# Optimization experiments

Hardware: AMD Instinct MI355X
Metric: run time of the kernel (lower is better)

The kernel has to match this reference:

```python
import jax, jax.numpy as jnp
import numpy as np
import math

S, B, D = 2048, 8, 256
HEADS = 8
DPROJ = 128
DFF = 1024
DH = DPROJ // HEADS  # 16


def _layernorm(x, g, b, eps=1e-5):
    mu = jnp.mean(x, axis=-1, keepdims=True)
    var = jnp.mean((x - mu) ** 2, axis=-1, keepdims=True)
    return (x - mu) * jax.lax.rsqrt(var + eps) * g + b


def setup_inputs() -> dict:
    key = jax.random.key(0)
    ks = jax.random.split(key, 16)
    s = 0.02
    return {
        "src": jax.random.normal(ks[0], (S, B, D), dtype=jnp.float32),
        "Wq": jax.random.normal(ks[1], (D, DPROJ), dtype=jnp.float32) * s,
        "bq": jnp.zeros((DPROJ,), dtype=jnp.float32),
        "Wk": jax.random.normal(ks[2], (D, DPROJ), dtype=jnp.float32) * s,
        "bk": jnp.zeros((DPROJ,), dtype=jnp.float32),
        "Wv": jax.random.normal(ks[3], (D, DPROJ), dtype=jnp.float32) * s,
        "bv": jnp.zeros((DPROJ,), dtype=jnp.float32),
        "Wo": jax.random.normal(ks[4], (DPROJ, D), dtype=jnp.float32) * s,
        "ln1_g": jnp.ones((D,), dtype=jnp.float32),
        "ln1_b": jnp.zeros((D,), dtype=jnp.float32),
        "W1": jax.random.normal(ks[5], (D, DFF), dtype=jnp.float32) * s,
        "b1": jnp.zeros((DFF,), dtype=jnp.float32),
        "W2": jax.random.normal(ks[6], (DFF, D), dtype=jnp.float32) * s,
        "b2": jnp.zeros((D,), dtype=jnp.float32),
        "ln2_g": jnp.ones((D,), dtype=jnp.float32),
        "ln2_b": jnp.zeros((D,), dtype=jnp.float32),
    }


def reference(src, Wq, bq, Wk, bk, Wv, bv, Wo, ln1_g, ln1_b, W1, b1, W2, b2, ln2_g, ln2_b):
    # src: (S, B, D)
    q = src @ Wq + bq  # (S, B, DPROJ)
    k = src @ Wk + bk
    v = src @ Wv + bv

    # _reshape_to_batches: (S, B, h*dh) -> (S, B*h, dh), then sdpa moves batch first
    def split_heads(x):
        return jnp.transpose(x.reshape(S, B * HEADS, DH), (1, 0, 2))  # (B*h, S, dh)

    qh, kh, vh = split_heads(q), split_heads(k), split_heads(v)
    scores = jnp.einsum('bid,bjd->bij', qh, kh) / math.sqrt(DH)  # (B*h, S, S)
    attn = jax.nn.softmax(scores, axis=-1)
    ctx = jnp.einsum('bij,bjd->bid', attn, vh)  # (B*h, S, dh)

    # _reshape_from_batches: (B*h, S, dh) -> (S, B, DPROJ)
    ctx = jnp.transpose(ctx, (1, 0, 2)).reshape(S, B, DPROJ)
    y = ctx @ Wo  # (S, B, D), no bias

    x = _layernorm(src + y, ln1_g, ln1_b)
    ffn = jax.nn.relu(x @ W1 + b1) @ W2 + b2
    return _layernorm(x + ffn, ln2_g, ln2_b)
```

## Files before the change

### kernel.cpp

```cpp
#include <hip/hip_runtime.h>
#include <math.h>

#define SLEN 2048
#define BATCH 8
#define DMODEL 256
#define HEADS 8
#define DPROJ 128
#define DFF 1024
#define DH 16
#define MROWS (SLEN*BATCH)

typedef unsigned short u16;
typedef unsigned int u32;
typedef __attribute__((ext_vector_type(8))) short short8;
typedef __attribute__((ext_vector_type(4))) float f32x4;
typedef __attribute__((ext_vector_type(4))) unsigned short u16x4;

__device__ __forceinline__ u16 f2bf(float x) {
    union { float f; u32 u; } v; v.f = x;
    u32 r = v.u + 0x7FFFu + ((v.u >> 16) & 1u);
    return (u16)(r >> 16);
}
__device__ __forceinline__ float bf2f(u16 h) {
    union { u32 u; float f; } v; v.u = ((u32)h) << 16;
    return v.f;
}
__device__ __forceinline__ float fexp2(float x) { return __builtin_amdgcn_exp2f(x); }
__device__ __forceinline__ u32 pack_bf(float lo, float hi) {
    union { float f; u32 u; } a, b; a.f = lo; b.f = hi;
    return __builtin_amdgcn_perm(b.u, a.u, 0x07060302u);
}
__device__ __forceinline__ void gld16(const u16* g, u16* l) {
    __builtin_amdgcn_global_load_lds(
        (const __attribute__((address_space(1))) void*)g,
        (__attribute__((address_space(3))) void*)l, 16, 0, 0);
}

__global__ void prep_kernel(const float* __restrict__ src, u16* __restrict__ srcb,
                            const float* __restrict__ Wq, const float* __restrict__ Wk,
                            const float* __restrict__ Wv, const float* __restrict__ Wo,
                            const float* __restrict__ W1, const float* __restrict__ W2,
                            u16* __restrict__ WqT, u16* __restrict__ WkT,
                            u16* __restrict__ WvT, u16* __restrict__ WoT,
                            u16* __restrict__ W1T, u16* __restrict__ W2T) {
    if (blockIdx.x < 4096) {
        int idx = (blockIdx.x * 256 + threadIdx.x) * 4;
        float4 v = *(const float4*)(src + idx);
        u16x4 o;
        o.x = f2bf(v.x); o.y = f2bf(v.y); o.z = f2bf(v.z); o.w = f2bf(v.w);
        *(u16x4*)(srcb + idx) = o;
        return;
    }
    int i = (blockIdx.x - 4096) * 256 + threadIdx.x;
    if (i < 32768) {
        int n = i >> 8, k = i & 255;
        WqT[i] = f2bf(Wq[k * 128 + n]);
    } else if (i < 65536) {
        int j = i - 32768; int n = j >> 8, k = j & 255;
        WkT[j] = f2bf(Wk[k * 128 + n]);
    } else if (i < 98304) {
        int j = i - 65536; int n = j >> 8, k = j & 255;
        WvT[j] = f2bf(Wv[k * 128 + n]);
    } else if (i < 131072) {
        int j = i - 98304; int n = j >> 7, k = j & 127;
        WoT[j] = f2bf(Wo[k * 256 + n]);
    } else if (i < 393216) {
        int j = i - 131072; int n = j >> 8, k = j & 255;
        W1T[j] = f2bf(W1[k * 1024 + n]);
    } else if (i < 655360) {
        int j = i - 393216; int n = j >> 10, k = j & 1023;
        W2T[j] = f2bf(W2[k * 256 + n]);
    }
}

template<int BN, bool RELU, bool HAS_BIAS, bool OUT_BF16>
__global__ void mfma_gemm(const u16* __restrict__ A, const u16* __restrict__ BT,
                          const float* __restrict__ bias, void* __restrict__ Cout,
                          int M, int N, int K) {
    constexpr int NJ = BN / 32;
    __shared__ __align__(16) u16 As[128 * 32];
    __shared__ __align__(16) u16 Bs[BN * 32];
    const int tid = threadIdx.x;
    const int row0 = blockIdx.x * 128;
    const int col0 = blockIdx.y * BN;
    const int w = tid >> 6, l = tid & 63;
    const int wr = (w & 1) * 64, wc = (w >> 1) * (BN / 2);
    const int lcol = l & 15, lrow = (l >> 4) * 4, g = l >> 4;
    const int sl = l >> 2;
    const int swc = ((l & 3) ^ (sl & 3)) * 8;
    const int fsw = (g ^ (lcol & 3)) * 8;

    const u16* Ag0 = A + (size_t)(row0 + 16 * w + sl) * K + swc;
    const u16* Ag1 = Ag0 + (size_t)64 * K;
    const u16* Bg0 = BT + (size_t)(col0 + 16 * w + sl) * K + swc;
    const u16* Bg1 = Bg0 + (size_t)64 * K;
    u16* lA0 = As + (16 * w) * 32;
    u16* lA1 = As + (16 * w + 64) * 32;
    u16* lB0 = Bs + (16 * w) * 32;
    u16* lB1 = Bs + (16 * w + 64) * 32;

    f32x4 acc[4][NJ] = {};
    for (int k0 = 0; k0 < K; k0 += 32) {
        gld16(Ag0 + k0, lA0);
        gld16(Ag1 + k0, lA1);
        gld16(Bg0 + k0, lB0);
        if (BN == 128) gld16(Bg1 + k0, lB1);
        __syncthreads();
        short8 af[4], bf[NJ];
        #pragma unroll
        for (int i = 0; i < 4; ++i)
            af[i] = *(const short8*)(As + (wr + i * 16 + lcol) * 32 + fsw);
        #pragma unroll
        for (int j = 0; j < NJ; ++j)
            bf[j] = *(const short8*)(Bs + (wc + j * 16 + lcol) * 32 + fsw);
        #pragma unroll
        for (int i = 0; i < 4; ++i)
            #pragma unroll
            for (int j = 0; j < NJ; ++j)
                acc[i][j] = __builtin_amdgcn_mfma_f32_16x16x32_bf16(
                    af[i], bf[j], acc[i][j], 0, 0, 0);
        __syncthreads();
    }
    float bv[NJ];
    #pragma unroll
    for (int j = 0; j < NJ; ++j)
        bv[j] = HAS_BIAS ? bias[col0 + wc + j * 16 + lcol] : 0.f;
    #pragma unroll
    for (int i = 0; i < 4; ++i) {
        #pragma unroll
        for (int r = 0; r < 4; ++r) {
            size_t grow = row0 + wr + i * 16 + lrow + r;
            #pragma unroll
            for (int j = 0; j < NJ; ++j) {
                int gcol = col0 + wc + j * 16 + lcol;
                float c = acc[i][j][r] + bv[j];
                if (RELU) c = fmaxf(c, 0.f);
                if (OUT_BF16) ((u16*)Cout)[grow * N + gcol] = f2bf(c);
                else          ((float*)Cout)[grow * N + gcol] = c;
            }
        }
    }
}

__global__ void qkv_mfma(const u16* __restrict__ A,
                         const u16* __restrict__ WqT, const u16* __restrict__ WkT,
                         const u16* __restrict__ WvT,
                         const float* __restrict__ bq, const float* __restrict__ bk,
                         const float* __restrict__ bv,
                         u16* __restrict__ qhp, u16* __restrict__ khp,
                         u16* __restrict__ vhb) {
    const int which = blockIdx.z;
    const u16* BT   = which == 0 ? WqT : (which == 1 ? WkT : WvT);
    const float* bs = which == 0 ? bq : (which == 1 ? bk : bv);
    const float scale = which == 0 ? 0.25f * 1.44269504f : 1.0f;
    __shared__ __align__(16) u16 As[128 * 32];
    __shared__ __align__(16) u16 Bs[128 * 32];
    const int tid = threadIdx.x;
    const int row0 = blockIdx.x * 128;
    const int w = tid >> 6, l = tid & 63;
    const int wr = (w & 1) * 64, wc = (w >> 1) * 64;
    const int lcol = l & 15, lrow = (l >> 4) * 4, g = l >> 4;
    const int sl = l >> 2;
    const int swc = ((l & 3) ^ (sl & 3)) * 8;
    const int fsw = (g ^ (lcol & 3)) * 8;

    const u16* Ag0 = A + (size_t)(row0 + 16 * w + sl) * DMODEL + swc;
    const u16* Ag1 = Ag0 + (size_t)64 * DMODEL;
    const u16* Bg0 = BT + (size_t)(16 * w + sl) * DMODEL + swc;
    const u16* Bg1 = Bg0 + (size_t)64 * DMODEL;
    u16* lA0 = As + (16 * w) * 32;
    u16* lA1 = As + (16 * w + 64) * 32;
    u16* lB0 = Bs + (16 * w) * 32;
    u16* lB1 = Bs + (16 * w + 64) * 32;

    f32x4 acc[4][4] = {};
    for (int k0 = 0; k0 < DMODEL; k0 += 32) {
        gld16(Ag0 + k0, lA0);
        gld16(Ag1 + k0, lA1);
        gld16(Bg0 + k0, lB0);
        gld16(Bg1 + k0, lB1);
        __syncthreads();
        short8 af[4], bf[4];
        #pragma unroll
        for (int i = 0; i < 4; ++i)
            af[i] = *(const short8*)(As + (wr + i * 16 + lcol) * 32 + fsw);
        #pragma unroll
        for (int j = 0; j < 4; ++j)
            bf[j] = *(const short8*)(Bs + (wc + j * 16 + lcol) * 32 + fsw);
        #pragma unroll
        for (int i = 0; i < 4; ++i)
            #pragma unroll
            for (int j = 0; j < 4; ++j)
                acc[i][j] = __builtin_amdgcn_mfma_f32_16x16x32_bf16(
                    af[i], bf[j], acc[i][j], 0, 0, 0);
        __syncthreads();
    }
    #pragma unroll
    for (int i = 0; i < 4; ++i) {
        #pragma unroll
        for (int r = 0; r < 4; ++r) {
            int grow = row0 + wr + i * 16 + lrow + r;
            int b = grow & 7, s = grow >> 3;
            #pragma unroll
            for (int j = 0; j < 4; ++j) {
                int gcol = wc + j * 16 + lcol;
                int h = gcol >> 4, d = gcol & 15;
                float c = acc[i][j][r] + bs[gcol];
                if (which == 2) {
                    vhb[((size_t)(b * 8 + h) * SLEN + s) * 16 + d] = f2bf(c);
                } else {
                    u16* base = (which == 0 ? qhp : khp)
                              + ((size_t)(b * 8 + h) * SLEN + s) * 32;
                    base[d] = f2bf(c * scale);
                    base[d + 16] = 0;
                }
            }
        }
    }
}

__global__ void transpose_v(const u16* __restrict__ vhb, u16* __restrict__ vT) {
    __shared__ u16 T[128 * 24];
    const int bh = blockIdx.y;
    const int c0 = blockIdx.x * 128;
    const int t = threadIdx.x;
    {
        int key = t >> 1, half = t & 1;
        *(uint4*)(T + key * 24 + half * 8) =
            *(const uint4*)(vhb + ((size_t)bh * SLEN + c0 + key) * 16 + half * 8);
    }
    __syncthreads();
    int d = t >> 4, k8 = (t & 15) * 8;
    u16x4 o0, o1;
    o0.x = T[(k8 + 0) * 24 + d]; o0.y = T[(k8 + 1) * 24 + d];
    o0.z = T[(k8 + 2) * 24 + d]; o0.w = T[(k8 + 3) * 24 + d];
    o1.x = T[(k8 + 4) * 24 + d]; o1.y = T[(k8 + 5) * 24 + d];
    o1.z = T[(k8 + 6) * 24 + d]; o1.w = T[(k8 + 7) * 24 + d];
    u16* dst = vT + ((size_t)bh * 16 + d) * SLEN + c0 + k8;
    *(u16x4*)dst = o0;
    *(u16x4*)(dst + 4) = o1;
}

__global__ __launch_bounds__(256, 4)
void attn_mfma(const u16* __restrict__ qg, const u16* __restrict__ kg,
               const u16* __restrict__ vT, u16* __restrict__ ctx) {
    __shared__ __align__(16) u16 Ps[2 * 4 * 32 * 76];
    const int bh = blockIdx.y;
    const int q0 = blockIdx.x * 128;
    const int tid = threadIdx.x;
    const int w = tid >> 6, l = tid & 63;
    const int qc = l & 15, g = l >> 4;
    u16* Pw0 = Ps + w * 2432;
    u16* Pw1 = Ps + 9728 + w * 2432;

    short8 qf[2];
    {
        const u16* qbase = qg + ((size_t)bh * SLEN + q0 + w * 32) * 32;
        qf[0] = *(const short8*)(qbase + qc * 32 + 8 * g);
        qf[1] = *(const short8*)(qbase + (16 + qc) * 32 + 8 * g);
    }
    const u16* kbase = kg + (size_t)bh * SLEN * 32;
    const u16* vbase = vT + ((size_t)bh * 16 + qc) * SLEN;

    f32x4 o_[2] = {};
    f32x4 ls[2] = {};
    const short one_bf = (short)0x3F80;
    short8 onesB = {one_bf, one_bf, one_bf, one_bf, one_bf, one_bf, one_bf, one_bf};

    #pragma unroll 2
    for (int kt = 0; kt < 32; ++kt) {
        const int k0 = kt * 64;
        u16* Pw = (kt & 1) ? Pw1 : Pw0;
        short8 kf[4], vf[2];
        #pragma unroll
        for (int kj = 0; kj < 4; ++kj)
            kf[kj] = *(const short8*)(kbase + (size_t)(k0 + kj * 16 + qc) * 32 + 8 * g);
        #pragma unroll
        for (int ks = 0; ks < 2; ++ks)
            vf[ks] = *(const short8*)(vbase + k0 + ks * 32 + 8 * g);

        f32x4 s_[4][2];
        #pragma unroll
        for (int kj = 0; kj < 4; ++kj)
            #pragma unroll
            for (int mi = 0; mi < 2; ++mi) {
                f32x4 z = {0.f, 0.f, 0.f, 0.f};
                s_[kj][mi] = __builtin_amdgcn_mfma_f32_16x16x32_bf16(
                    kf[kj], qf[mi], z, 0, 0, 0);
            }
        #pragma unroll
        for (int mi = 0; mi < 2; ++mi)
            #pragma unroll
            for (int kj = 0; kj < 4; ++kj) {
                f32x4 sv = s_[kj][mi];
                uint2 dd;
                dd.x = pack_bf(fexp2(sv[0]), fexp2(sv[1]));
                dd.y = pack_bf(fexp2(sv[2]), fexp2(sv[3]));
                *(uint2*)(Pw + (mi * 16 + qc) * 76 + kj * 16 + 4 * g) = dd;
            }
        #pragma unroll
        for (int ks = 0; ks < 2; ++ks) {
            #pragma unroll
            for (int mi = 0; mi < 2; ++mi) {
                const u16* rp = Pw + (mi * 16 + qc) * 76 + ks * 32 + 8 * g;
                union { uint2 q[2]; short8 v; } ap;
                ap.q[0] = *(const uint2*)rp;
                ap.q[1] = *(const uint2*)(rp + 4);
                o_[mi] = __builtin_amdgcn_mfma_f32_16x16x32_bf16(ap.v, vf[ks], o_[mi], 0, 0, 0);
                ls[mi] = __builtin_amdgcn_mfma_f32_16x16x32_bf16(ap.v, onesB, ls[mi], 0, 0, 0);
            }
        }
    }
    const int b = bh >> 3, h = bh & 7;
    #pragma unroll
    for (int mi = 0; mi < 2; ++mi)
        #pragma unroll
        for (int r = 0; r < 4; ++r) {
            int qrow = q0 + w * 32 + mi * 16 + 4 * g + r;
            ctx[((size_t)qrow * BATCH + b) * DPROJ + h * DH + qc] =
                f2bf(o_[mi][r] / ls[mi][r]);
        }
}

__global__ void ln1_kernel(const float* __restrict__ src, const u16* __restrict__ y,
                           const float* __restrict__ g, const float* __restrict__ bb,
                           u16* __restrict__ xb) {
    const int w = threadIdx.x >> 6, l = threadIdx.x & 63;
    const int row = blockIdx.x * 4 + w;
    const int c = l * 4;
    size_t base = (size_t)row * DMODEL;
    float4 s4 = *(const float4*)(src + base + c);
    u16x4 y4 = *(const u16x4*)(y + base + c);
    float v[4] = { s4.x + bf2f(y4.x), s4.y + bf2f(y4.y),
                   s4.z + bf2f(y4.z), s4.w + bf2f(y4.w) };
    float sum = v[0] + v[1] + v[2] + v[3];
    float ss  = v[0]*v[0] + v[1]*v[1] + v[2]*v[2] + v[3]*v[3];
    #pragma unroll
    for (int off = 1; off < 64; off <<= 1) {
        sum += __shfl_xor(sum, off);
        ss  += __shfl_xor(ss, off);
    }
    float mu = sum * (1.0f / 256.0f);
    float var = ss * (1.0f / 256.0f) - mu * mu;
    float rs = rsqrtf(var + 1e-5f);
    float4 g4 = *(const float4*)(g + c);
    float4 b4 = *(const float4*)(bb + c);
    u16x4 o;
    o.x = f2bf((v[0] - mu) * rs * g4.x + b4.x);
    o.y = f2bf((v[1] - mu) * rs * g4.y + b4.y);
    o.z = f2bf((v[2] - mu) * rs * g4.z + b4.z);
    o.w = f2bf((v[3] - mu) * rs * g4.w + b4.w);
    *(u16x4*)(xb + base + c) = o;
}

__global__ void ln2_kernel(const u16* __restrict__ x, const u16* __restrict__ f,
                           const float* __restrict__ g, const float* __restrict__ bb,
                           float* __restrict__ out) {
    const int w = threadIdx.x >> 6, l = threadIdx.x & 63;
    const int row = blockIdx.x * 4 + w;
    const int c = l * 4;
    size_t base = (size_t)row * DMODEL;
    u16x4 x4 = *(const u16x4*)(x + base + c);
    u16x4 f4 = *(const u16x4*)(f + base + c);
    float v[4] = { bf2f(x4.x) + bf2f(f4.x), bf2f(x4.y) + bf2f(f4.y),
                   bf2f(x4.z) + bf2f(f4.z), bf2f(x4.w) + bf2f(f4.w) };
    float sum = v[0] + v[1] + v[2] + v[3];
    float ss  = v[0]*v[0] + v[1]*v[1] + v[2]*v[2] + v[3]*v[3];
    #pragma unroll
    for (int off = 1; off < 64; off <<= 1) {
        sum += __shfl_xor(sum, off);
        ss  += __shfl_xor(ss, off);
    }
    float mu = sum * (1.0f / 256.0f);
    float var = ss * (1.0f / 256.0f) - mu * mu;
    float rs = rsqrtf(var + 1e-5f);
    float4 g4 = *(const float4*)(g + c);
    float4 b4 = *(const float4*)(bb + c);
    float4 o;
    o.x = (v[0] - mu) * rs * g4.x + b4.x;
    o.y = (v[1] - mu) * rs * g4.y + b4.y;
    o.z = (v[2] - mu) * rs * g4.z + b4.z;
    o.w = (v[3] - mu) * rs * g4.w + b4.w;
    *(float4*)(out + base + c) = o;
}

extern "C" void kernel_launch(void* const* d_in, const int* in_sizes, int n_in,
                              void* d_out, int out_size, void* d_ws, size_t ws_size,
                              hipStream_t stream) {
    const float* src = (const float*)d_in[0];
    const float* Wq  = (const float*)d_in[1];
    const float* bq  = (const float*)d_in[2];
    const float* Wk  = (const float*)d_in[3];
    const float* bk  = (const float*)d_in[4];
    const float* Wv  = (const float*)d_in[5];
    const float* bv  = (const float*)d_in[6];
    const float* Wo  = (const float*)d_in[7];
    const float* g1  = (const float*)d_in[8];
    const float* be1 = (const float*)d_in[9];
    const float* W1  = (const float*)d_in[10];
    const float* b1  = (const float*)d_in[11];
    const float* W2  = (const float*)d_in[12];
    const float* b2  = (const float*)d_in[13];
    const float* g2  = (const float*)d_in[14];
    const float* be2 = (const float*)d_in[15];
    char* ws = (char*)d_ws;
    float* out = (float*)d_out;

    u16* qhp  = (u16*)(ws + 0);
    u16* khp  = (u16*)(ws + 8388608);
    u16* vhb  = (u16*)(ws + 16777216);
    u16* vT   = (u16*)(ws + 20971520);
    u16* ctxb = (u16*)(ws + 25165824);
    u16* yb   = (u16*)(ws + 29360128);
    u16* hb   = (u16*)(ws + 0);
    u16* xb   = (u16*)(ws + 37748736);
    u16* fb   = (u16*)(ws + 46137344);
    u16* srcb = (u16*)(ws + 54525952);
    u16* WqT  = (u16*)(ws + 62914560);
    u16* WkT  = (u16*)(ws + 62980096);
    u16* WvT  = (u16*)(ws + 63045632);
    u16* WoT  = (u16*)(ws + 63111168);
    u16* W1T  = (u16*)(ws + 63176704);
    u16* W2T  = (u16*)(ws + 63700992);

    prep_kernel<<<6656, 256, 0, stream>>>(src, srcb, Wq, Wk, Wv, Wo, W1, W2,
                                          WqT, WkT, WvT, WoT, W1T, W2T);
    qkv_mfma<<<dim3(128, 1, 3), 256, 0, stream>>>(srcb, WqT, WkT, WvT,
                                                  bq, bk, bv, qhp, khp, vhb);
    transpose_v<<<dim3(16, 64), 256, 0, stream>>>(vhb, vT);
    attn_mfma<<<dim3(16, 64), 256, 0, stream>>>(qhp, khp, vT, ctxb);
    mfma_gemm<64, false, false, true><<<dim3(128, 4), 256, 0, stream>>>(
        ctxb, WoT, nullptr, yb, MROWS, DMODEL, DPROJ);
    ln1_kernel<<<MROWS / 4, 256, 0, stream>>>(src, yb, g1, be1, xb);
    mfma_gemm<128, true, true, true><<<dim3(128, 8), 256, 0, stream>>>(
        xb, W1T, b1, hb, MROWS, DFF, DMODEL);
    mfma_gemm<64, false, true, true><<<dim3(128, 4), 256, 0, stream>>>(
        hb, W2T, b2, fb, MROWS, DMODEL, DFF);
    ln2_kernel<<<MROWS / 4, 256, 0, stream>>>(xb, fb, g2, be2, out);
}
```

Measured before the change: 231.4 us.

## Switch attention to 32x32x16 MFMA with ones-augmented V for row sums

Rewrites the attention kernel to use 32x32x16 bf16 MFMA on unpadded 16-wide Q/K, removing the zero padding to K=32 that the 16x16x32 path needed. V is transposed into a 32-row augmented layout whose row 16 holds ones, so the softmax denominator comes out of the same PV MFMA instead of a separate ones-matrix MFMA. K fragments are prefetched one tile ahead, and the epilogue stages results through LDS for vectorized normalized stores. This wastes half of the output MFMA columns on padding and adds an LDS round trip in the epilogue.

```diff
diff --git a/kernel.cpp b/kernel.cpp
--- a/kernel.cpp
+++ b/kernel.cpp
@@ -14,6 +14,7 @@
 typedef unsigned int u32;
 typedef __attribute__((ext_vector_type(8))) short short8;
 typedef __attribute__((ext_vector_type(4))) float f32x4;
+typedef __attribute__((ext_vector_type(16))) float f32x16;
 typedef __attribute__((ext_vector_type(4))) unsigned short u16x4;
 
 __device__ __forceinline__ u16 f2bf(float x) {
@@ -152,6 +153,7 @@
     const int which = blockIdx.z;
     const u16* BT   = which == 0 ? WqT : (which == 1 ? WkT : WvT);
     const float* bs = which == 0 ? bq : (which == 1 ? bk : bv);
+    u16* outp       = which == 0 ? qhp : (which == 1 ? khp : vhb);
     const float scale = which == 0 ? 0.25f * 1.44269504f : 1.0f;
     __shared__ __align__(16) u16 As[128 * 32];
     __shared__ __align__(16) u16 Bs[128 * 32];
@@ -206,20 +208,13 @@
                 int gcol = wc + j * 16 + lcol;
                 int h = gcol >> 4, d = gcol & 15;
                 float c = acc[i][j][r] + bs[gcol];
-                if (which == 2) {
-                    vhb[((size_t)(b * 8 + h) * SLEN + s) * 16 + d] = f2bf(c);
-                } else {
-                    u16* base = (which == 0 ? qhp : khp)
-                              + ((size_t)(b * 8 + h) * SLEN + s) * 32;
-                    base[d] = f2bf(c * scale);
-                    base[d + 16] = 0;
-                }
+                outp[((size_t)(b * 8 + h) * SLEN + s) * 16 + d] = f2bf(c * scale);
             }
         }
     }
 }
 
-__global__ void transpose_v(const u16* __restrict__ vhb, u16* __restrict__ vT) {
+__global__ void transpose_v(const u16* __restrict__ vhb, u16* __restrict__ va) {
     __shared__ u16 T[128 * 24];
     const int bh = blockIdx.y;
     const int c0 = blockIdx.x * 128;
@@ -236,90 +231,89 @@
     o0.z = T[(k8 + 2) * 24 + d]; o0.w = T[(k8 + 3) * 24 + d];
     o1.x = T[(k8 + 4) * 24 + d]; o1.y = T[(k8 + 5) * 24 + d];
     o1.z = T[(k8 + 6) * 24 + d]; o1.w = T[(k8 + 7) * 24 + d];
-    u16* dst = vT + ((size_t)bh * 16 + d) * SLEN + c0 + k8;
+    u16* dst = va + ((size_t)bh * 32 + d) * SLEN + c0 + k8;
     *(u16x4*)dst = o0;
     *(u16x4*)(dst + 4) = o1;
+    if (t < 16) {
+        u16x4 ones = { (u16)0x3F80, (u16)0x3F80, (u16)0x3F80, (u16)0x3F80 };
+        u16* od = va + ((size_t)bh * 32 + 16) * SLEN + c0 + t * 8;
+        *(u16x4*)od = ones;
+        *(u16x4*)(od + 4) = ones;
+    }
 }
 
 __global__ __launch_bounds__(256, 4)
 void attn_mfma(const u16* __restrict__ qg, const u16* __restrict__ kg,
-               const u16* __restrict__ vT, u16* __restrict__ ctx) {
-    __shared__ __align__(16) u16 Ps[2 * 4 * 32 * 76];
+               const u16* __restrict__ va, u16* __restrict__ ctx) {
+    __shared__ __align__(16) u16 Ps[4 * 2 * 32 * 72];
     const int bh = blockIdx.y;
     const int q0 = blockIdx.x * 128;
     const int tid = threadIdx.x;
     const int w = tid >> 6, l = tid & 63;
-    const int qc = l & 15, g = l >> 4;
-    u16* Pw0 = Ps + w * 2432;
-    u16* Pw1 = Ps + 9728 + w * 2432;
-
-    short8 qf[2];
-    {
-        const u16* qbase = qg + ((size_t)bh * SLEN + q0 + w * 32) * 32;
-        qf[0] = *(const short8*)(qbase + qc * 32 + 8 * g);
-        qf[1] = *(const short8*)(qbase + (16 + qc) * 32 + 8 * g);
-    }
-    const u16* kbase = kg + (size_t)bh * SLEN * 32;
-    const u16* vbase = vT + ((size_t)bh * 16 + qc) * SLEN;
-
-    f32x4 o_[2] = {};
-    f32x4 ls[2] = {};
-    const short one_bf = (short)0x3F80;
-    short8 onesB = {one_bf, one_bf, one_bf, one_bf, one_bf, one_bf, one_bf, one_bf};
-
-    #pragma unroll 2
+    const int n = l & 31, h5 = l >> 5;
+    u16* Pbase = Ps + w * (2 * 32 * 72);
+
+    const short8 qf = *(const short8*)(
+        qg + ((size_t)bh * SLEN + q0 + w * 32 + n) * 16 + h5 * 8);
+    const u16* kb = kg + (size_t)bh * SLEN * 16;
+    const u16* vb = va + ((size_t)bh * 32 + n) * SLEN + h5 * 8;
+
+    f32x16 oacc = {};
+
+    short8 kf0 = *(const short8*)(kb + (size_t)n * 16 + h5 * 8);
+    short8 kf1 = *(const short8*)(kb + (size_t)(32 + n) * 16 + h5 * 8);
+
     for (int kt = 0; kt < 32; ++kt) {
         const int k0 = kt * 64;
-        u16* Pw = (kt & 1) ? Pw1 : Pw0;
-        short8 kf[4], vf[2];
-        #pragma unroll
-        for (int kj = 0; kj < 4; ++kj)
-            kf[kj] = *(const short8*)(kbase + (size_t)(k0 + kj * 16 + qc) * 32 + 8 * g);
-        #pragma unroll
-        for (int ks = 0; ks < 2; ++ks)
-            vf[ks] = *(const short8*)(vbase + k0 + ks * 32 + 8 * g);
-
-        f32x4 s_[4][2];
-        #pragma unroll
-        for (int kj = 0; kj < 4; ++kj)
-            #pragma unroll
-            for (int mi = 0; mi < 2; ++mi) {
-                f32x4 z = {0.f, 0.f, 0.f, 0.f};
-                s_[kj][mi] = __builtin_amdgcn_mfma_f32_16x16x32_bf16(
-                    kf[kj], qf[mi], z, 0, 0, 0);
-            }
-        #pragma unroll
-        for (int mi = 0; mi < 2; ++mi)
-            #pragma unroll
-            for (int kj = 0; kj < 4; ++kj) {
-                f32x4 sv = s_[kj][mi];
-                uint2 dd;
-                dd.x = pack_bf(fexp2(sv[0]), fexp2(sv[1]));
-                dd.y = pack_bf(fexp2(sv[2]), fexp2(sv[3]));
-                *(uint2*)(Pw + (mi * 16 + qc) * 76 + kj * 16 + 4 * g) = dd;
-            }
-        #pragma unroll
-        for (int ks = 0; ks < 2; ++ks) {
-            #pragma unroll
-            for (int mi = 0; mi < 2; ++mi) {
-                const u16* rp = Pw + (mi * 16 + qc) * 76 + ks * 32 + 8 * g;
-                union { uint2 q[2]; short8 v; } ap;
-                ap.q[0] = *(const uint2*)rp;
-                ap.q[1] = *(const uint2*)(rp + 4);
-                o_[mi] = __builtin_amdgcn_mfma_f32_16x16x32_bf16(ap.v, vf[ks], o_[mi], 0, 0, 0);
-                ls[mi] = __builtin_amdgcn_mfma_f32_16x16x32_bf16(ap.v, onesB, ls[mi], 0, 0, 0);
-            }
+        u16* Pw = Pbase + (kt & 1) * (32 * 72);
+        short8 vf[4];
+        #pragma unroll
+        for (int st = 0; st < 4; ++st)
+            vf[st] = *(const short8*)(vb + k0 + st * 16);
+        f32x16 z = {};
+        f32x16 s0 = __builtin_amdgcn_mfma_f32_32x32x16_bf16(kf0, qf, z, 0, 0, 0);
+        f32x16 s1 = __builtin_amdgcn_mfma_f32_32x32x16_bf16(kf1, qf, z, 0, 0, 0);
+        const int kn = (kt < 31) ? (k0 + 64) : 0;
+        kf0 = *(const short8*)(kb + (size_t)(kn + n) * 16 + h5 * 8);
+        kf1 = *(const short8*)(kb + (size_t)(kn + 32 + n) * 16 + h5 * 8);
+        #pragma unroll
+        for (int r4 = 0; r4 < 4; ++r4) {
+            uint2 d0, d1;
+            d0.x = pack_bf(fexp2(s0[r4 * 4 + 0]), fexp2(s0[r4 * 4 + 1]));
+            d0.y = pack_bf(fexp2(s0[r4 * 4 + 2]), fexp2(s0[r4 * 4 + 3]));
+            d1.x = pack_bf(fexp2(s1[r4 * 4 + 0]), fexp2(s1[r4 * 4 + 1]));
+            d1.y = pack_bf(fexp2(s1[r4 * 4 + 2]), fexp2(s1[r4 * 4 + 3]));
+            int kbase = 8 * r4 + 4 * h5;
+            *(uint2*)(Pw + n * 72 + kbase) = d0;
+            *(uint2*)(Pw + n * 72 + 32 + kbase) = d1;
         }
-    }
+        #pragma unroll
+        for (int st = 0; st < 4; ++st) {
+            short8 ap = *(const short8*)(Pw + n * 72 + st * 16 + h5 * 8);
+            oacc = __builtin_amdgcn_mfma_f32_32x32x16_bf16(ap, vf[st], oacc, 0, 0, 0);
+        }
+    }
+    float* Ob = (float*)Pbase;
+    #pragma unroll
+    for (int r = 0; r < 16; ++r) {
+        int q = (r & 3) + 8 * (r >> 2) + 4 * h5;
+        if (n <= 16) Ob[q * 36 + n] = oacc[r];
+    }
+    __syncthreads();
+    const int q = l >> 1, half = l & 1;
+    f32x4 o0 = *(const f32x4*)(Ob + q * 36 + half * 8);
+    f32x4 o1 = *(const f32x4*)(Ob + q * 36 + half * 8 + 4);
+    float rcpL = 1.0f / Ob[q * 36 + 16];
+    u16x4 pa, pb;
+    pa.x = f2bf(o0[0] * rcpL); pa.y = f2bf(o0[1] * rcpL);
+    pa.z = f2bf(o0[2] * rcpL); pa.w = f2bf(o0[3] * rcpL);
+    pb.x = f2bf(o1[0] * rcpL); pb.y = f2bf(o1[1] * rcpL);
+    pb.z = f2bf(o1[2] * rcpL); pb.w = f2bf(o1[3] * rcpL);
     const int b = bh >> 3, h = bh & 7;
-    #pragma unroll
-    for (int mi = 0; mi < 2; ++mi)
-        #pragma unroll
-        for (int r = 0; r < 4; ++r) {
-            int qrow = q0 + w * 32 + mi * 16 + 4 * g + r;
-            ctx[((size_t)qrow * BATCH + b) * DPROJ + h * DH + qc] =
-                f2bf(o_[mi][r] / ls[mi][r]);
-        }
+    const int qrow = q0 + w * 32 + q;
+    u16* dst = ctx + ((size_t)qrow * BATCH + b) * DPROJ + h * DH + half * 8;
+    *(u16x4*)dst = pa;
+    *(u16x4*)(dst + 4) = pb;
 }
 
 __global__ void ln1_kernel(const float* __restrict__ src, const u16* __restrict__ y,
@@ -407,28 +401,28 @@
     float* out = (float*)d_out;
 
     u16* qhp  = (u16*)(ws + 0);
-    u16* khp  = (u16*)(ws + 8388608);
-    u16* vhb  = (u16*)(ws + 16777216);
-    u16* vT   = (u16*)(ws + 20971520);
-    u16* ctxb = (u16*)(ws + 25165824);
-    u16* yb   = (u16*)(ws + 29360128);
+    u16* khp  = (u16*)(ws + 4194304);
+    u16* vhb  = (u16*)(ws + 8388608);
+    u16* vaug = (u16*)(ws + 12582912);
+    u16* ctxb = (u16*)(ws + 20971520);
+    u16* yb   = (u16*)(ws + 25165824);
     u16* hb   = (u16*)(ws + 0);
-    u16* xb   = (u16*)(ws + 37748736);
-    u16* fb   = (u16*)(ws + 46137344);
-    u16* srcb = (u16*)(ws + 54525952);
-    u16* WqT  = (u16*)(ws + 62914560);
-    u16* WkT  = (u16*)(ws + 62980096);
-    u16* WvT  = (u16*)(ws + 63045632);
-    u16* WoT  = (u16*)(ws + 63111168);
-    u16* W1T  = (u16*)(ws + 63176704);
-    u16* W2T  = (u16*)(ws + 63700992);
+    u16* xb   = (u16*)(ws + 33554432);
+    u16* fb   = (u16*)(ws + 41943040);
+    u16* srcb = (u16*)(ws + 50331648);
+    u16* WqT  = (u16*)(ws + 58720256);
+    u16* WkT  = (u16*)(ws + 58785792);
+    u16* WvT  = (u16*)(ws + 58851328);
+    u16* WoT  = (u16*)(ws + 58916864);
+    u16* W1T  = (u16*)(ws + 58982400);
+    u16* W2T  = (u16*)(ws + 59506688);
 
     prep_kernel<<<6656, 256, 0, stream>>>(src, srcb, Wq, Wk, Wv, Wo, W1, W2,
                                           WqT, WkT, WvT, WoT, W1T, W2T);
     qkv_mfma<<<dim3(128, 1, 3), 256, 0, stream>>>(srcb, WqT, WkT, WvT,
                                                   bq, bk, bv, qhp, khp, vhb);
-    transpose_v<<<dim3(16, 64), 256, 0, stream>>>(vhb, vT);
-    attn_mfma<<<dim3(16, 64), 256, 0, stream>>>(qhp, khp, vT, ctxb);
+    transpose_v<<<dim3(16, 64), 256, 0, stream>>>(vhb, vaug);
+    attn_mfma<<<dim3(16, 64), 256, 0, stream>>>(qhp, khp, vaug, ctxb);
     mfma_gemm<64, false, false, true><<<dim3(128, 4), 256, 0, stream>>>(
         ctxb, WoT, nullptr, yb, MROWS, DMODEL, DPROJ);
     ln1_kernel<<<MROWS / 4, 256, 0, stream>>>(src, yb, g1, be1, xb);
```

Measured after the change: 240.4 us. 3.9% more time.
